# Kernel tuning notes

Hardware: AMD Instinct MI355X
Metric: run time of the kernel (lower is better)

## Reference

```python
import jax, jax.numpy as jnp
import numpy as np

U = 64       # LTC units / motor neurons
I = 128      # sensory (input) size
O = 15       # output_size
UNFOLDS = 4  # ode_unfolds
EPS = 1e-8   # ncps LTCCell epsilon


def setup_inputs() -> dict:
    key = jax.random.key(0)
    ks = jax.random.split(key, 16)
    B, T = 512, 512
    u = lambda k, shp, lo, hi: jax.random.uniform(k, shp, jnp.float32, lo, hi)
    sign = lambda k, shp: jnp.where(jax.random.bernoulli(k, 0.5, shp), 1.0, -1.0).astype(jnp.float32)
    return {
        "x": jax.random.normal(ks[0], (B, T, I), jnp.float32),
        # affine input mapping
        "input_w": jnp.ones((I,), jnp.float32),
        "input_b": jnp.zeros((I,), jnp.float32),
        # sensory synapses (I -> U)
        "sensory_w": u(ks[1], (I, U), 0.001, 1.0),
        "sensory_mu": u(ks[2], (I, U), 0.3, 0.8),
        "sensory_sigma": u(ks[3], (I, U), 3.0, 8.0),
        "sensory_erev": sign(ks[4], (I, U)),
        # recurrent synapses (U -> U)
        "w": u(ks[5], (U, U), 0.001, 1.0),
        "mu": u(ks[6], (U, U), 0.3, 0.8),
        "sigma": u(ks[7], (U, U), 3.0, 8.0),
        "erev": sign(ks[8], (U, U)),
        # per-neuron params
        "gleak": u(ks[9], (U,), 0.001, 1.0),
        "vleak": u(ks[10], (U,), -0.2, 0.2),
        "cm": u(ks[11], (U,), 0.4, 0.6),
        # affine output mapping
        "output_w": jnp.ones((U,), jnp.float32),
        "output_b": jnp.zeros((U,), jnp.float32),
        # LayerNorm + fc head
        "ln_w": jnp.ones((U,), jnp.float32),
        "ln_b": jnp.zeros((U,), jnp.float32),
        "fc_w": jax.random.normal(ks[12], (O, U), jnp.float32) * 0.05,
        "fc_b": jnp.zeros((O,), jnp.float32),
    }


def reference(x, input_w, input_b, sensory_w, sensory_mu, sensory_sigma, sensory_erev,
              w, mu, sigma, erev, gleak, vleak, cm, output_w, output_b,
              ln_w, ln_b, fc_w, fc_b):
    B = x.shape[0]
    sp = jax.nn.softplus
    # implicit_param_constraints=True -> softplus on w, sensory_w, gleak, cm
    w_pos = sp(w)
    sw_pos = sp(sensory_w)
    gleak_p = sp(gleak)
    cm_t = sp(cm) / (1.0 / UNFOLDS)  # elapsed_time = 1.0

    @jax.checkpoint
    def step(v, xt):
        inp = xt * input_w + input_b                                   # (B, I)
        s_act = sw_pos * jax.nn.sigmoid(sensory_sigma * (inp[:, :, None] - sensory_mu))  # (B, I, U)
        w_num_s = jnp.sum(s_act * sensory_erev, axis=1)                # (B, U)
        w_den_s = jnp.sum(s_act, axis=1)                               # (B, U)

        def unfold(v, _):
            w_act = w_pos * jax.nn.sigmoid(sigma * (v[:, :, None] - mu))  # (B, U, U)
            num = cm_t * v + gleak_p * vleak + jnp.sum(w_act * erev, axis=1) + w_num_s
            den = cm_t + gleak_p + jnp.sum(w_act, axis=1) + w_den_s
            return num / (den + EPS), None

        v, _ = jax.lax.scan(unfold, v, None, length=UNFOLDS)
        return v, None

    v0 = jnp.zeros((B, U), x.dtype)
    v_last, _ = jax.lax.scan(step, v0, jnp.swapaxes(x, 0, 1))  # scan over T
    # affine output mapping of the LTC (motor = all units for FullyConnected)
    h = v_last * output_w + output_b                               # (B, U)
    # LayerNorm (eps=1e-5) -- dropout is identity in eval
    mean = jnp.mean(h, axis=-1, keepdims=True)
    var = jnp.var(h, axis=-1, keepdims=True)
    h = (h - mean) * jax.lax.rsqrt(var + 1e-5) * ln_w + ln_b
    return h @ fc_w.T + fc_b                                       # (B, O)
```

## Files before the change

kernel.cpp:

```cpp
#include <hip/hip_runtime.h>


#define NB 512
#define NT 512
#define NI 128
#define NU 64
#define NO 15
#define L2E 1.44269504088896340736f

__device__ __forceinline__ float bcastf(float v, int lane) {
  return __int_as_float(__builtin_amdgcn_readlane(__float_as_int(v), lane));
}

__device__ __forceinline__ float wsum64(float x) {
#pragma unroll
  for (int m = 32; m >= 1; m >>= 1) x += __shfl_xor(x, m, 64);
  return x;
}

__device__ __forceinline__ float softplus_f(float x) {
  return log1pf(expf(x));
}

__device__ __forceinline__ float sigm_term(float a, float vb, float c) {
  float z = fmaf(a, vb, c);
  float e = __builtin_amdgcn_exp2f(z);
  return __builtin_amdgcn_rcpf(1.0f + e);
}

__global__ __launch_bounds__(256, 1) void ltc_fused(
    const float* __restrict__ x,
    const float* __restrict__ input_w, const float* __restrict__ input_b,
    const float* __restrict__ sensory_w, const float* __restrict__ sensory_mu,
    const float* __restrict__ sensory_sigma, const float* __restrict__ sensory_erev,
    const float* __restrict__ w_, const float* __restrict__ mu_,
    const float* __restrict__ sigma_, const float* __restrict__ erev_,
    const float* __restrict__ gleak, const float* __restrict__ vleak,
    const float* __restrict__ cm,
    const float* __restrict__ output_w, const float* __restrict__ output_b,
    const float* __restrict__ ln_w, const float* __restrict__ ln_b,
    const float* __restrict__ fc_w, const float* __restrict__ fc_b,
    float* __restrict__ out)
{
  const int b    = blockIdx.x;
  const int tid  = threadIdx.x;
  const int wv   = tid >> 6;
  const int lane = tid & 63;

  __shared__ float2 xbuf[4][4][NU];

  float sa[32], sc[32], swe[32];
#pragma unroll
  for (int k = 0; k < 32; ++k) {
    const int idx = (32 * wv + k) * NU + lane;
    const float ss = sensory_sigma[idx];
    const float sm = sensory_mu[idx];
    const float sw = softplus_f(sensory_w[idx]);
    const float se = sensory_erev[idx];
    sa[k]  = -L2E * ss;
    sc[k]  =  L2E * ss * sm;
    swe[k] = sw * se;
  }
  float ra[16], rc[16], rwe[16];
#pragma unroll
  for (int k = 0; k < 16; ++k) {
    const int idx = (16 * wv + k) * NU + lane;
    const float sg = sigma_[idx];
    const float m  = mu_[idx];
    const float ww = softplus_f(w_[idx]);
    const float ev = erev_[idx];
    ra[k]  = -L2E * sg;
    rc[k]  =  L2E * sg * m;
    rwe[k] = ww * ev;
  }

  const float glp   = softplus_f(gleak[lane]);
  const float cmt   = softplus_f(cm[lane]) * 4.0f;
  const float glvl  = glp * vleak[lane];
  const float dbase = cmt + glp + 1e-8f;

  const int ii = 32 * wv + (lane & 31);
  const float iw = input_w[ii];
  const float ib = input_b[ii];

  float v = 0.0f;
  const float* xp = x + (size_t)b * NT * NI + ii;
  float xv = xp[0];

#pragma unroll 1
  for (int t = 0; t < NT; ++t) {
    const int tn = (t + 1 < NT) ? (t + 1) : t;
    const float xv_next = xp[(size_t)tn * NI];
    const float inp = fmaf(xv, iw, ib);

    float ns0=0.f, ns1=0.f, ns2=0.f, ns3=0.f;
    float ds0=0.f, ds1=0.f, ds2=0.f, ds3=0.f;
#pragma unroll
    for (int k = 0; k < 32; k += 4) {
      { float s = sigm_term(sa[k+0], bcastf(inp, k+0), sc[k+0]);
        ns0 = fmaf(swe[k+0], s, ns0); ds0 = fmaf(fabsf(swe[k+0]), s, ds0); }
      { float s = sigm_term(sa[k+1], bcastf(inp, k+1), sc[k+1]);
        ns1 = fmaf(swe[k+1], s, ns1); ds1 = fmaf(fabsf(swe[k+1]), s, ds1); }
      { float s = sigm_term(sa[k+2], bcastf(inp, k+2), sc[k+2]);
        ns2 = fmaf(swe[k+2], s, ns2); ds2 = fmaf(fabsf(swe[k+2]), s, ds2); }
      { float s = sigm_term(sa[k+3], bcastf(inp, k+3), sc[k+3]);
        ns3 = fmaf(swe[k+3], s, ns3); ds3 = fmaf(fabsf(swe[k+3]), s, ds3); }
    }
    const float wns = (ns0 + ns1) + (ns2 + ns3);
    const float wds = (ds0 + ds1) + (ds2 + ds3);

#pragma unroll
    for (int u = 0; u < 4; ++u) {
      float rn0=0.f, rn1=0.f, rn2=0.f, rn3=0.f;
      float rd0=0.f, rd1=0.f, rd2=0.f, rd3=0.f;
      const int i0 = 16 * wv;
#pragma unroll
      for (int k = 0; k < 16; k += 4) {
        { float s = sigm_term(ra[k+0], bcastf(v, i0+k+0), rc[k+0]);
          rn0 = fmaf(rwe[k+0], s, rn0); rd0 = fmaf(fabsf(rwe[k+0]), s, rd0); }
        { float s = sigm_term(ra[k+1], bcastf(v, i0+k+1), rc[k+1]);
          rn1 = fmaf(rwe[k+1], s, rn1); rd1 = fmaf(fabsf(rwe[k+1]), s, rd1); }
        { float s = sigm_term(ra[k+2], bcastf(v, i0+k+2), rc[k+2]);
          rn2 = fmaf(rwe[k+2], s, rn2); rd2 = fmaf(fabsf(rwe[k+2]), s, rd2); }
        { float s = sigm_term(ra[k+3], bcastf(v, i0+k+3), rc[k+3]);
          rn3 = fmaf(rwe[k+3], s, rn3); rd3 = fmaf(fabsf(rwe[k+3]), s, rd3); }
      }
      const float np = ((rn0 + rn1) + (rn2 + rn3)) + wns;
      const float dp = ((rd0 + rd1) + (rd2 + rd3)) + wds;
      xbuf[u][wv][lane] = make_float2(np, dp);
      __syncthreads();
      const float2 p0 = xbuf[u][0][lane];
      const float2 p1 = xbuf[u][1][lane];
      const float2 p2 = xbuf[u][2][lane];
      const float2 p3 = xbuf[u][3][lane];
      const float num = fmaf(cmt, v, glvl) + ((p0.x + p1.x) + (p2.x + p3.x));
      const float den = dbase + ((p0.y + p1.y) + (p2.y + p3.y));
      v = num * __builtin_amdgcn_rcpf(den);
    }
    xv = xv_next;
  }

  if (wv == 0) {
    const float h    = fmaf(v, output_w[lane], output_b[lane]);
    const float mean = wsum64(h) * (1.0f / 64.0f);
    const float d    = h - mean;
    const float var  = wsum64(d * d) * (1.0f / 64.0f);
    const float hn   = d * rsqrtf(var + 1e-5f) * ln_w[lane] + ln_b[lane];
#pragma unroll
    for (int o = 0; o < NO; ++o) {
      const float p = wsum64(hn * fc_w[o * NU + lane]);
      if (lane == 0) out[b * NO + o] = p + fc_b[o];
    }
  }
}

extern "C" void kernel_launch(void* const* d_in, const int* in_sizes, int n_in,
                              void* d_out, int out_size, void* d_ws, size_t ws_size,
                              hipStream_t stream) {
  const float* x             = (const float*)d_in[0];
  const float* input_w       = (const float*)d_in[1];
  const float* input_b       = (const float*)d_in[2];
  const float* sensory_w     = (const float*)d_in[3];
  const float* sensory_mu    = (const float*)d_in[4];
  const float* sensory_sigma = (const float*)d_in[5];
  const float* sensory_erev  = (const float*)d_in[6];
  const float* w_            = (const float*)d_in[7];
  const float* mu_           = (const float*)d_in[8];
  const float* sigma_        = (const float*)d_in[9];
  const float* erev_         = (const float*)d_in[10];
  const float* gleak         = (const float*)d_in[11];
  const float* vleak         = (const float*)d_in[12];
  const float* cm            = (const float*)d_in[13];
  const float* output_w      = (const float*)d_in[14];
  const float* output_b      = (const float*)d_in[15];
  const float* ln_w          = (const float*)d_in[16];
  const float* ln_b          = (const float*)d_in[17];
  const float* fc_w          = (const float*)d_in[18];
  const float* fc_b          = (const float*)d_in[19];
  float* out = (float*)d_out;

  ltc_fused<<<dim3(NB), dim3(256), 0, stream>>>(
      x, input_w, input_b, sensory_w, sensory_mu, sensory_sigma, sensory_erev,
      w_, mu_, sigma_, erev_, gleak, vleak, cm, output_w, output_b,
      ln_w, ln_b, fc_w, fc_b, out);
}
```

Before: 2.121 ms.

## Software-pipeline sensory synapse sum for next timestep across unfold barriers

Folds the input affine mapping into the precomputed sensory sigmoid coefficients, which removes one FMA per timestep. It also restructures the time loop so the sensory sum for step t+1 is computed in four slices, one placed after each unfold's barrier, while step t's recurrent unfolds run. The aim is to hide barrier and dependency latency by interleaving independent exp and rcp work with the serial unfold chain. In exchange there is a prologue, x is prefetched two steps ahead, and the last iteration does redundant work on a clamped index.

```diff
diff --git a/kernel.cpp b/kernel.cpp
--- a/kernel.cpp
+++ b/kernel.cpp
@@ -52,13 +52,18 @@
   float sa[32], sc[32], swe[32];
 #pragma unroll
   for (int k = 0; k < 32; ++k) {
-    const int idx = (32 * wv + k) * NU + lane;
-    const float ss = sensory_sigma[idx];
-    const float sm = sensory_mu[idx];
-    const float sw = softplus_f(sensory_w[idx]);
-    const float se = sensory_erev[idx];
-    sa[k]  = -L2E * ss;
-    sc[k]  =  L2E * ss * sm;
+    const int i   = 32 * wv + k;
+    const int idx = i * NU + lane;
+    const float ss  = sensory_sigma[idx];
+    const float sm  = sensory_mu[idx];
+    const float sw  = softplus_f(sensory_w[idx]);
+    const float se  = sensory_erev[idx];
+    const float iwk = input_w[i];
+    const float ibk = input_b[i];
+    const float a = -L2E * ss;
+    const float c =  L2E * ss * sm;
+    sa[k]  = a * iwk;
+    sc[k]  = fmaf(a, ibk, c);
     swe[k] = sw * se;
   }
   float ra[16], rc[16], rwe[16];
@@ -80,34 +85,36 @@
   const float dbase = cmt + glp + 1e-8f;
 
   const int ii = 32 * wv + (lane & 31);
-  const float iw = input_w[ii];
-  const float ib = input_b[ii];
 
   float v = 0.0f;
   const float* xp = x + (size_t)b * NT * NI + ii;
-  float xv = xp[0];
+
+  float wns, wds;
+  {
+    const float xv0 = xp[0];
+    float n0=0.f, n1=0.f, n2=0.f, n3=0.f;
+    float d0=0.f, d1=0.f, d2=0.f, d3=0.f;
+#pragma unroll
+    for (int k = 0; k < 32; k += 4) {
+      { float s = sigm_term(sa[k+0], bcastf(xv0, k+0), sc[k+0]);
+        n0 = fmaf(swe[k+0], s, n0); d0 = fmaf(fabsf(swe[k+0]), s, d0); }
+      { float s = sigm_term(sa[k+1], bcastf(xv0, k+1), sc[k+1]);
+        n1 = fmaf(swe[k+1], s, n1); d1 = fmaf(fabsf(swe[k+1]), s, d1); }
+      { float s = sigm_term(sa[k+2], bcastf(xv0, k+2), sc[k+2]);
+        n2 = fmaf(swe[k+2], s, n2); d2 = fmaf(fabsf(swe[k+2]), s, d2); }
+      { float s = sigm_term(sa[k+3], bcastf(xv0, k+3), sc[k+3]);
+        n3 = fmaf(swe[k+3], s, n3); d3 = fmaf(fabsf(swe[k+3]), s, d3); }
+    }
+    wns = (n0 + n1) + (n2 + n3);
+    wds = (d0 + d1) + (d2 + d3);
+  }
+  float xv_next = xp[NI];
 
 #pragma unroll 1
   for (int t = 0; t < NT; ++t) {
-    const int tn = (t + 1 < NT) ? (t + 1) : t;
-    const float xv_next = xp[(size_t)tn * NI];
-    const float inp = fmaf(xv, iw, ib);
-
-    float ns0=0.f, ns1=0.f, ns2=0.f, ns3=0.f;
-    float ds0=0.f, ds1=0.f, ds2=0.f, ds3=0.f;
-#pragma unroll
-    for (int k = 0; k < 32; k += 4) {
-      { float s = sigm_term(sa[k+0], bcastf(inp, k+0), sc[k+0]);
-        ns0 = fmaf(swe[k+0], s, ns0); ds0 = fmaf(fabsf(swe[k+0]), s, ds0); }
-      { float s = sigm_term(sa[k+1], bcastf(inp, k+1), sc[k+1]);
-        ns1 = fmaf(swe[k+1], s, ns1); ds1 = fmaf(fabsf(swe[k+1]), s, ds1); }
-      { float s = sigm_term(sa[k+2], bcastf(inp, k+2), sc[k+2]);
-        ns2 = fmaf(swe[k+2], s, ns2); ds2 = fmaf(fabsf(swe[k+2]), s, ds2); }
-      { float s = sigm_term(sa[k+3], bcastf(inp, k+3), sc[k+3]);
-        ns3 = fmaf(swe[k+3], s, ns3); ds3 = fmaf(fabsf(swe[k+3]), s, ds3); }
-    }
-    const float wns = (ns0 + ns1) + (ns2 + ns3);
-    const float wds = (ds0 + ds1) + (ds2 + ds3);
+    const int tpp = (t + 2 < NT) ? (t + 2) : (NT - 1);
+    const float xv_pp = xp[(size_t)tpp * NI];
+    float nsn0=0.f, nsn1=0.f, dsn0=0.f, dsn1=0.f;
 
 #pragma unroll
     for (int u = 0; u < 4; ++u) {
@@ -133,11 +140,25 @@
       const float2 p1 = xbuf[u][1][lane];
       const float2 p2 = xbuf[u][2][lane];
       const float2 p3 = xbuf[u][3][lane];
+      {
+        const int kk = 8 * u;
+#pragma unroll
+        for (int j = 0; j < 8; j += 2) {
+          { float s = sigm_term(sa[kk+j],   bcastf(xv_next, kk+j),   sc[kk+j]);
+            nsn0 = fmaf(swe[kk+j],   s, nsn0);
+            dsn0 = fmaf(fabsf(swe[kk+j]),   s, dsn0); }
+          { float s = sigm_term(sa[kk+j+1], bcastf(xv_next, kk+j+1), sc[kk+j+1]);
+            nsn1 = fmaf(swe[kk+j+1], s, nsn1);
+            dsn1 = fmaf(fabsf(swe[kk+j+1]), s, dsn1); }
+        }
+      }
       const float num = fmaf(cmt, v, glvl) + ((p0.x + p1.x) + (p2.x + p3.x));
       const float den = dbase + ((p0.y + p1.y) + (p2.y + p3.y));
       v = num * __builtin_amdgcn_rcpf(den);
     }
-    xv = xv_next;
+    wns = nsn0 + nsn1;
+    wds = dsn0 + dsn1;
+    xv_next = xv_pp;
   }
 
   if (wv == 0) {
```

Result: faster. 2.066 ms (-2.6%).
